# Kernel optimization log

Measured on AMD Instinct MI355X. Metric: run time of the kernel, lower is better.

Reference implementation:

```python
import jax, jax.numpy as jnp
import numpy as np

B, H, E = 16, 4096, 512
N_MODES = 24  # len(index_q), permutation of range(48//2)


def setup_inputs() -> dict:
    key = jax.random.key(0)
    ks = jax.random.split(key, 7)
    s = 1.0 / np.sqrt(E)
    inp = {
        "x": jax.random.normal(ks[0], (B, H, E), jnp.float32),
        "Wq": jax.random.normal(ks[1], (E, E), jnp.float32) * s,
        "bq": jax.random.normal(ks[2], (E,), jnp.float32) * s,
        "Wk": jax.random.normal(ks[3], (E, E), jnp.float32) * s,
        "bk": jax.random.normal(ks[4], (E,), jnp.float32) * s,
        "Wv": jax.random.normal(ks[5], (E, E), jnp.float32) * s,
        "bv": jax.random.normal(ks[6], (E,), jnp.float32) * s,
        # shuffled permutation of range(24), as in the module __init__
        "index_q": jnp.asarray(np.random.RandomState(0).permutation(N_MODES), jnp.int32),
    }
    return inp


def reference(x, Wq, bq, Wk, bk, Wv, bv, index_q):
    # nn.Linear: y = x @ W.T + b
    Q = x @ Wq.T + bq
    K = x @ Wk.T + bk
    V = x @ Wv.T + bv  # computed but unused downstream (faithful to original bug)
    del V

    # rFFT over feature dim, gather selected frequency modes (vectorized,
    # replacing the original per-index Python loops)
    xq_ft = jnp.fft.rfft(Q, axis=-1)[:, :, index_q]          # [B,H,24] complex
    xk_ft = jnp.fft.rfft(K, axis=-1)[:, :, index_q]          # [B,H,24]
    xv_ft = xk_ft                                            # original uses rfft(K) for V too

    # cross-frequency attention: contract over H (no conjugation, as torch.einsum)
    xqk_ft = jnp.einsum('bhx,bhy->bxy', xq_ft, xk_ft)        # [B,24,24] complex
    att = jax.nn.softmax(jnp.abs(xqk_ft), axis=-1)           # real [B,24,24]
    att_c = jax.lax.complex(att, jnp.zeros_like(att))
    xqkv_ft = jnp.einsum('bxy,bhy->bhx', att_c, xv_ft)       # [B,H,24]

    # scatter selected modes back into the full spectrum, inverse rFFT
    n_freq = E // 2 + 1
    out_ft = jnp.zeros((x.shape[0], x.shape[1], n_freq), jnp.complex64)
    out_ft = out_ft.at[:, :, index_q].set(xqkv_ft)
    out = jnp.fft.irfft(out_ft, n=E, axis=-1)                # [B,H,E] real
    return out.astype(x.dtype)
```

## Files before the change

kernel.cpp:

```cpp
#include <hip/hip_runtime.h>
#include <stdint.h>

#define E_DIM 512
#define NM 24
#define NC 48
#define NCOL 96
#define B_DIM 16
#define H_DIM 4096
#define NROWS (B_DIM * H_DIM)
#define NPAIR 576

typedef _Float16 half8 __attribute__((ext_vector_type(8)));
typedef float f32x4 __attribute__((ext_vector_type(4)));

__global__ __launch_bounds__(512)
void k_build(const float* __restrict__ Wq, const float* __restrict__ Wk,
             const float* __restrict__ bq, const float* __restrict__ bk,
             const int* __restrict__ idxq,
             _Float16* __restrict__ Cth, _Float16* __restrict__ Ctl,
             float* __restrict__ dvec, float* __restrict__ M) {
  const int t = threadIdx.x;
  const int bid = blockIdx.x;
  if (bid >= NCOL) {
    const int c = bid - NCOL;
    const int j = c >> 1, p = c & 1;
    const int f = idxq[j];
    const float w = (f == 0 ? 1.0f : 2.0f) * (1.0f / (float)E_DIM);
    float s, cc;
    sincospif((float)((f * t) & (E_DIM - 1)) * (1.0f / 256.0f), &s, &cc);
    M[c * E_DIM + t] = p ? (-w * s) : (w * cc);
    return;
  }
  __shared__ float tw[E_DIM];
  const int mat = bid / NC;
  const int c = bid - mat * NC;
  const int j = c >> 1, p = c & 1;
  const int f = idxq[j];
  {
    float s, cc;
    sincospif((float)((f * t) & (E_DIM - 1)) * (1.0f / 256.0f), &s, &cc);
    tw[t] = p ? -s : cc;
  }
  __syncthreads();
  const float* __restrict__ W = mat ? Wk : Wq;
  float acc = 0.0f;
#pragma unroll 8
  for (int o = 0; o < E_DIM; ++o)
    acc = fmaf(W[o * E_DIM + t], tw[o], acc);
  const _Float16 hi = (_Float16)acc;
  Cth[bid * E_DIM + t] = hi;
  Ctl[bid * E_DIM + t] = (_Float16)(acc - (float)hi);
  if (t < 64) {
    const float* __restrict__ bv = mat ? bk : bq;
    float ba = 0.0f;
#pragma unroll
    for (int r = 0; r < 8; ++r) {
      const int o = r * 64 + t;
      ba = fmaf(bv[o], tw[o], ba);
    }
#pragma unroll
    for (int off = 32; off > 0; off >>= 1)
      ba += __shfl_down(ba, off, 64);
    if (t == 0) dvec[bid] = ba;
  }
}

#define GSTR 100
__global__ __launch_bounds__(256)
void k_gemmG(const float* __restrict__ x, const _Float16* __restrict__ Cth,
             const _Float16* __restrict__ Ctl, const float* __restrict__ dvec,
             float* __restrict__ Gk, float* __restrict__ Sp) {
  __shared__ __align__(16) float gs[128 * GSTR];
  const int t = threadIdx.x;
  const int lane = t & 63;
  const int wv = t >> 6;
  const int rb = blockIdx.x * 128 + wv * 32;
  const int lm = lane & 15;
  const int lk = lane >> 4;
  f32x4 acc[6][2];
#pragma unroll
  for (int mt = 0; mt < 6; ++mt)
#pragma unroll
    for (int nt = 0; nt < 2; ++nt) acc[mt][nt] = (f32x4){0.f, 0.f, 0.f, 0.f};

  float4 xv[2][2];
#pragma unroll
  for (int nt = 0; nt < 2; ++nt) {
    const float* __restrict__ xp = &x[(size_t)(rb + nt * 16 + lm) * E_DIM + lk * 8];
    xv[nt][0] = *(const float4*)xp;
    xv[nt][1] = *(const float4*)(xp + 4);
  }

  for (int k0 = 0; k0 < E_DIM; k0 += 32) {
    half8 xh[2], xl[2];
#pragma unroll
    for (int nt = 0; nt < 2; ++nt) {
      const float vv[8] = {xv[nt][0].x, xv[nt][0].y, xv[nt][0].z, xv[nt][0].w,
                           xv[nt][1].x, xv[nt][1].y, xv[nt][1].z, xv[nt][1].w};
#pragma unroll
      for (int i = 0; i < 8; ++i) {
        const _Float16 h = (_Float16)vv[i];
        xh[nt][i] = h;
        xl[nt][i] = (_Float16)(vv[i] - (float)h);
      }
    }
    if (k0 + 32 < E_DIM) {
      const int kn = k0 + 32;
#pragma unroll
      for (int nt = 0; nt < 2; ++nt) {
        const float* __restrict__ xp =
            &x[(size_t)(rb + nt * 16 + lm) * E_DIM + kn + lk * 8];
        xv[nt][0] = *(const float4*)xp;
        xv[nt][1] = *(const float4*)(xp + 4);
      }
    }
#pragma unroll
    for (int mt = 0; mt < 6; ++mt) {
      const int arow = mt * 16 + lm;
      const half8 Ah = *(const half8*)&Cth[arow * E_DIM + k0 + lk * 8];
      const half8 Al = *(const half8*)&Ctl[arow * E_DIM + k0 + lk * 8];
#pragma unroll
      for (int nt = 0; nt < 2; ++nt) {
        acc[mt][nt] = __builtin_amdgcn_mfma_f32_16x16x32_f16(Ah, xh[nt], acc[mt][nt], 0, 0, 0);
        acc[mt][nt] = __builtin_amdgcn_mfma_f32_16x16x32_f16(Al, xh[nt], acc[mt][nt], 0, 0, 0);
        acc[mt][nt] = __builtin_amdgcn_mfma_f32_16x16x32_f16(Ah, xl[nt], acc[mt][nt], 0, 0, 0);
      }
    }
  }
#pragma unroll
  for (int mt = 0; mt < 6; ++mt) {
    const int c0 = mt * 16 + lk * 4;
    const float4 bias = *(const float4*)&dvec[c0];
#pragma unroll
    for (int nt = 0; nt < 2; ++nt) {
      acc[mt][nt][0] += bias.x;
      acc[mt][nt][1] += bias.y;
      acc[mt][nt][2] += bias.z;
      acc[mt][nt][3] += bias.w;
      if (mt >= 3) {
        const int r = rb + nt * 16 + lm;
        float4 st;
        st.x = acc[mt][nt][0]; st.y = acc[mt][nt][1];
        st.z = acc[mt][nt][2]; st.w = acc[mt][nt][3];
        *(float4*)&Gk[(size_t)r * NC + (c0 - NC)] = st;
      }
    }
  }
#pragma unroll
  for (int mt = 0; mt < 6; ++mt) {
    const int c0 = mt * 16 + lk * 4;
#pragma unroll
    for (int nt = 0; nt < 2; ++nt) {
      const int lrow = wv * 32 + nt * 16 + lm;
      float4 st;
      st.x = acc[mt][nt][0]; st.y = acc[mt][nt][1];
      st.z = acc[mt][nt][2]; st.w = acc[mt][nt][3];
      *(float4*)&gs[lrow * GSTR + c0] = st;
    }
  }
  __syncthreads();
#pragma unroll
  for (int r = 0; r < 3; ++r) {
    const int i = t + r * 256;
    if (i < NPAIR) {
      const int xx = i / NM, yy = i - xx * NM;
      float ar = 0.f, ai = 0.f;
      for (int h = 0; h < 128; ++h) {
        const float2 q = *(const float2*)&gs[h * GSTR + 2 * xx];
        const float2 k = *(const float2*)&gs[h * GSTR + NC + 2 * yy];
        ar += q.x * k.x - q.y * k.y;
        ai += q.x * k.y + q.y * k.x;
      }
      ((float2*)Sp)[(size_t)blockIdx.x * NPAIR + i] = make_float2(ar, ai);
    }
  }
}

__global__ __launch_bounds__(576)
void k_att(const float* __restrict__ Sp, float* __restrict__ att) {
  __shared__ float mag[NPAIR];
  __shared__ float ex[NPAIR];
  const int t = threadIdx.x;
  const int b = blockIdx.x;
  float sre = 0.0f, sim = 0.0f;
  const float2* in2 = (const float2*)Sp;
  for (int hc = 0; hc < 32; ++hc) {
    const float2 v = in2[(size_t)(b * 32 + hc) * NPAIR + t];
    sre += v.x; sim += v.y;
  }
  mag[t] = sqrtf(sre * sre + sim * sim);
  __syncthreads();
  const int xx = t / NM;
  float m = -1e30f;
  for (int k = 0; k < NM; ++k) m = fmaxf(m, mag[xx * NM + k]);
  const float e = expf(mag[t] - m);
  ex[t] = e;
  __syncthreads();
  float s = 0.0f;
  for (int k = 0; k < NM; ++k) s += ex[xx * NM + k];
  att[b * NPAIR + t] = e / s;
}

#define ZOB 128
#define ZON 256
__global__ __launch_bounds__(512)
void k_zout(const float* __restrict__ Gk, const float* __restrict__ M,
            const float* __restrict__ att, float* __restrict__ out) {
  __shared__ __align__(16) float ms[NC * ZON];
  __shared__ __align__(16) float zs[NC][ZOB + 4];
  __shared__ float at[NPAIR];
  const int t = threadIdx.x;
  const int row0 = (blockIdx.x >> 1) * ZOB;
  const int e0 = (blockIdx.x & 1) * ZON;
  const int b = row0 >> 12;
  float4 mv[6];
#pragma unroll
  for (int r = 0; r < 6; ++r) {
    const int idx = r * 512 + t;
    const int k = idx >> 6, ec = idx & 63;
    mv[r] = *(const float4*)&M[k * E_DIM + e0 + ec * 4];
  }
  at[t] = att[b * NPAIR + t];
  if (t < 64) at[512 + t] = att[b * NPAIR + 512 + t];
  __syncthreads();
#pragma unroll
  for (int r = 0; r < 6; ++r) {
    const int idx = r * 512 + t;
    *(float4*)&ms[idx * 4] = mv[r];
  }
  const int zrow = t >> 2;
  const int xg = t & 3;
  float gk[NC];
  {
    const float4* gk4 = (const float4*)&Gk[(size_t)(row0 + zrow) * NC];
#pragma unroll
    for (int i = 0; i < 12; ++i) {
      const float4 v = gk4[i];
      gk[i * 4 + 0] = v.x; gk[i * 4 + 1] = v.y;
      gk[i * 4 + 2] = v.z; gk[i * 4 + 3] = v.w;
    }
  }
  float z[12];
#pragma unroll
  for (int j = 0; j < 6; ++j) {
    const int xx = xg * 6 + j;
    float zr = 0.0f, zi = 0.0f;
#pragma unroll
    for (int y = 0; y < NM; ++y) {
      const float a = at[xx * NM + y];
      zr = fmaf(a, gk[2 * y], zr);
      zi = fmaf(a, gk[2 * y + 1], zi);
    }
    z[2 * j] = zr; z[2 * j + 1] = zi;
  }
#pragma unroll
  for (int s = 0; s < 12; ++s) zs[xg * 12 + s][zrow] = z[s];
  __syncthreads();
  const int rr = t >> 4;
  const int cg = t & 15;
  float acc[4][16];
#pragma unroll
  for (int a = 0; a < 4; ++a)
#pragma unroll
    for (int c = 0; c < 16; ++c) acc[a][c] = 0.0f;
#pragma unroll 4
  for (int kk = 0; kk < NC; ++kk) {
    const float4 zv = *(const float4*)&zs[kk][rr * 4];
    const float4 m0 = *(const float4*)&ms[kk * ZON + cg * 8 + 0];
    const float4 m1 = *(const float4*)&ms[kk * ZON + cg * 8 + 4];
    const float4 m2 = *(const float4*)&ms[kk * ZON + cg * 8 + 128];
    const float4 m3 = *(const float4*)&ms[kk * ZON + cg * 8 + 132];
    const float zr[4] = {zv.x, zv.y, zv.z, zv.w};
    const float mr[16] = {m0.x, m0.y, m0.z, m0.w, m1.x, m1.y, m1.z, m1.w,
                          m2.x, m2.y, m2.z, m2.w, m3.x, m3.y, m3.z, m3.w};
#pragma unroll
    for (int a = 0; a < 4; ++a)
#pragma unroll
      for (int c = 0; c < 16; ++c)
        acc[a][c] = fmaf(zr[a], mr[c], acc[a][c]);
  }
#pragma unroll
  for (int a = 0; a < 4; ++a) {
    const int row = row0 + rr * 4 + a;
    float4 v0, v1, v2, v3;
    v0.x = acc[a][0];  v0.y = acc[a][1];  v0.z = acc[a][2];  v0.w = acc[a][3];
    v1.x = acc[a][4];  v1.y = acc[a][5];  v1.z = acc[a][6];  v1.w = acc[a][7];
    v2.x = acc[a][8];  v2.y = acc[a][9];  v2.z = acc[a][10]; v2.w = acc[a][11];
    v3.x = acc[a][12]; v3.y = acc[a][13]; v3.z = acc[a][14]; v3.w = acc[a][15];
    float* o = &out[(size_t)row * E_DIM + e0 + cg * 8];
    *(float4*)(o + 0)   = v0;
    *(float4*)(o + 4)   = v1;
    *(float4*)(o + 128) = v2;
    *(float4*)(o + 132) = v3;
  }
}

extern "C" void kernel_launch(void* const* d_in, const int* in_sizes, int n_in,
                              void* d_out, int out_size, void* d_ws, size_t ws_size,
                              hipStream_t stream) {
  const float* x  = (const float*)d_in[0];
  const float* Wq = (const float*)d_in[1];
  const float* bq = (const float*)d_in[2];
  const float* Wk = (const float*)d_in[3];
  const float* bk = (const float*)d_in[4];
  const int* idxq = (const int*)d_in[7];
  float* out = (float*)d_out;
  float* ws = (float*)d_ws;

  _Float16* Cth = (_Float16*)ws;
  _Float16* Ctl = (_Float16*)(ws + 24576);
  float* dv  = ws + 49152;
  float* M   = ws + 49280;
  float* att = ws + 73856;
  float* Sp  = ws + 83072;
  float* Gk  = ws + 672896;

  k_build<<<NCOL + NC, 512, 0, stream>>>(Wq, Wk, bq, bk, idxq, Cth, Ctl, dv, M);
  k_gemmG<<<NROWS / 128, 256, 0, stream>>>(x, Cth, Ctl, dv, Gk, Sp);
  k_att<<<B_DIM, 576, 0, stream>>>(Sp, att);
  k_zout<<<(NROWS / ZOB) * (E_DIM / ZON), 512, 0, stream>>>(Gk, M, att, out);
}
```

Before: 377.4 us.

## Stage x and C tiles into LDS via async global_load_lds double buffering

The GEMM kernel now copies each 32-wide k-slice of x and of the hi/lo fp16 coefficient matrices into a double-buffered shared-memory tile using direct global-to-LDS loads. The next slice is prefetched while MFMAs run on the current one. Before, every wave read the coefficient matrices from global memory itself and x went through registers. This spreads global traffic across the block and overlaps loads with compute, at the cost of a __syncthreads per k-step and more shared memory, which may reduce occupancy.

Measured after the change: 356.1 us. 1.06x faster.

```diff
diff --git a/kernel.cpp b/kernel.cpp
--- a/kernel.cpp
+++ b/kernel.cpp
@@ -12,6 +12,12 @@
 
 typedef _Float16 half8 __attribute__((ext_vector_type(8)));
 typedef float f32x4 __attribute__((ext_vector_type(4)));
+
+__device__ __forceinline__ void gload16(const void* g, void* l) {
+  __builtin_amdgcn_global_load_lds(
+      (const __attribute__((address_space(1))) uint32_t*)g,
+      (__attribute__((address_space(3))) uint32_t*)l, 16, 0, 0);
+}
 
 __global__ __launch_bounds__(512)
 void k_build(const float* __restrict__ Wq, const float* __restrict__ Wk,
@@ -66,59 +72,83 @@
 }
 
 #define GSTR 100
+#define TILE_B 28672
 __global__ __launch_bounds__(256)
 void k_gemmG(const float* __restrict__ x, const _Float16* __restrict__ Cth,
              const _Float16* __restrict__ Ctl, const float* __restrict__ dvec,
              float* __restrict__ Gk, float* __restrict__ Sp) {
-  __shared__ __align__(16) float gs[128 * GSTR];
+  __shared__ __align__(16) uint8_t smem[2 * TILE_B];
   const int t = threadIdx.x;
   const int lane = t & 63;
   const int wv = t >> 6;
-  const int rb = blockIdx.x * 128 + wv * 32;
+  const int rb = blockIdx.x * 128;
+  const int wrow0 = wv * 32;
   const int lm = lane & 15;
   const int lk = lane >> 4;
+
+  const char* srcp[7];
+  int ksc[7];
+  int ldso[7];
+#pragma unroll
+  for (int j = 0; j < 7; ++j) {
+    const int c = wv * 7 + j;
+    ldso[j] = c * 1024;
+    if (c < 16) {
+      const int xlk = c >> 2;
+      const int r = (c & 3) * 32 + (lane >> 1);
+      const int h = lane & 1;
+      srcp[j] = (const char*)(x + (size_t)(rb + r) * E_DIM + xlk * 8 + h * 4);
+      ksc[j] = 4;
+    } else {
+      const int g = (c - 16) * 64 + lane;
+      const int part = g / 384;
+      const int rem = g - part * 384;
+      const int clk = rem / 96;
+      const int row = rem - clk * 96;
+      srcp[j] = (const char*)((part ? Ctl : Cth) + row * E_DIM + clk * 8);
+      ksc[j] = 2;
+    }
+  }
+
   f32x4 acc[6][2];
 #pragma unroll
   for (int mt = 0; mt < 6; ++mt)
 #pragma unroll
     for (int nt = 0; nt < 2; ++nt) acc[mt][nt] = (f32x4){0.f, 0.f, 0.f, 0.f};
 
-  float4 xv[2][2];
-#pragma unroll
-  for (int nt = 0; nt < 2; ++nt) {
-    const float* __restrict__ xp = &x[(size_t)(rb + nt * 16 + lm) * E_DIM + lk * 8];
-    xv[nt][0] = *(const float4*)xp;
-    xv[nt][1] = *(const float4*)(xp + 4);
-  }
-
-  for (int k0 = 0; k0 < E_DIM; k0 += 32) {
+#pragma unroll
+  for (int j = 0; j < 7; ++j)
+    gload16(srcp[j], smem + ldso[j]);
+  __syncthreads();
+
+  for (int kt = 0; kt < 16; ++kt) {
+    const int par = kt & 1;
+    if (kt < 15) {
+      const int kn = (kt + 1) * 32;
+#pragma unroll
+      for (int j = 0; j < 7; ++j)
+        gload16(srcp[j] + kn * ksc[j], smem + (par ^ 1) * TILE_B + ldso[j]);
+    }
+    const float* xb = (const float*)(smem + par * TILE_B);
+    const _Float16* cb = (const _Float16*)(smem + par * TILE_B + 16384);
     half8 xh[2], xl[2];
 #pragma unroll
     for (int nt = 0; nt < 2; ++nt) {
-      const float vv[8] = {xv[nt][0].x, xv[nt][0].y, xv[nt][0].z, xv[nt][0].w,
-                           xv[nt][1].x, xv[nt][1].y, xv[nt][1].z, xv[nt][1].w};
+      const float* xp = xb + lk * 1024 + (wrow0 + nt * 16 + lm) * 8;
+      const float4 a = *(const float4*)xp;
+      const float4 b = *(const float4*)(xp + 4);
+      const float vv[8] = {a.x, a.y, a.z, a.w, b.x, b.y, b.z, b.w};
 #pragma unroll
       for (int i = 0; i < 8; ++i) {
-        const _Float16 h = (_Float16)vv[i];
-        xh[nt][i] = h;
-        xl[nt][i] = (_Float16)(vv[i] - (float)h);
+        const _Float16 hh = (_Float16)vv[i];
+        xh[nt][i] = hh;
+        xl[nt][i] = (_Float16)(vv[i] - (float)hh);
       }
     }
-    if (k0 + 32 < E_DIM) {
-      const int kn = k0 + 32;
-#pragma unroll
-      for (int nt = 0; nt < 2; ++nt) {
-        const float* __restrict__ xp =
-            &x[(size_t)(rb + nt * 16 + lm) * E_DIM + kn + lk * 8];
-        xv[nt][0] = *(const float4*)xp;
-        xv[nt][1] = *(const float4*)(xp + 4);
-      }
-    }
 #pragma unroll
     for (int mt = 0; mt < 6; ++mt) {
-      const int arow = mt * 16 + lm;
-      const half8 Ah = *(const half8*)&Cth[arow * E_DIM + k0 + lk * 8];
-      const half8 Al = *(const half8*)&Ctl[arow * E_DIM + k0 + lk * 8];
+      const half8 Ah = *(const half8*)(cb + lk * 768 + (mt * 16 + lm) * 8);
+      const half8 Al = *(const half8*)(cb + 3072 + lk * 768 + (mt * 16 + lm) * 8);
 #pragma unroll
       for (int nt = 0; nt < 2; ++nt) {
         acc[mt][nt] = __builtin_amdgcn_mfma_f32_16x16x32_f16(Ah, xh[nt], acc[mt][nt], 0, 0, 0);
@@ -126,7 +156,10 @@
         acc[mt][nt] = __builtin_amdgcn_mfma_f32_16x16x32_f16(Ah, xl[nt], acc[mt][nt], 0, 0, 0);
       }
     }
-  }
+    __syncthreads();
+  }
+
+  float* gs = (float*)smem;
 #pragma unroll
   for (int mt = 0; mt < 6; ++mt) {
     const int c0 = mt * 16 + lk * 4;
@@ -137,24 +170,12 @@
       acc[mt][nt][1] += bias.y;
       acc[mt][nt][2] += bias.z;
       acc[mt][nt][3] += bias.w;
-      if (mt >= 3) {
-        const int r = rb + nt * 16 + lm;
-        float4 st;
-        st.x = acc[mt][nt][0]; st.y = acc[mt][nt][1];
-        st.z = acc[mt][nt][2]; st.w = acc[mt][nt][3];
-        *(float4*)&Gk[(size_t)r * NC + (c0 - NC)] = st;
-      }
-    }
-  }
-#pragma unroll
-  for (int mt = 0; mt < 6; ++mt) {
-    const int c0 = mt * 16 + lk * 4;
-#pragma unroll
-    for (int nt = 0; nt < 2; ++nt) {
-      const int lrow = wv * 32 + nt * 16 + lm;
+      const int lrow = wrow0 + nt * 16 + lm;
       float4 st;
       st.x = acc[mt][nt][0]; st.y = acc[mt][nt][1];
       st.z = acc[mt][nt][2]; st.w = acc[mt][nt][3];
+      if (mt >= 3)
+        *(float4*)&Gk[(size_t)(rb + lrow) * NC + (c0 - NC)] = st;
       *(float4*)&gs[lrow * GSTR + c0] = st;
     }
   }
```
